# Performance work log

Measured on AMD Instinct MI355X. Metric: run time of the kernel, lower is better.

Reference implementation:

```python
import jax, jax.numpy as jnp
import numpy as np

N_ITEMS = 80001
D = 128
K = 20
HOP = 2
ROUTING_ITER = 4
SAMPLE = 12
B = 256
S = 50


def layer_norm(x, g, b, eps=1e-5):
    mu = jnp.mean(x, -1, keepdims=True)
    var = jnp.var(x, -1, keepdims=True)
    return (x - mu) * jax.lax.rsqrt(var + eps) * g + b


def routing_agg(x, nb0):
    # NeighborRoutingAgg (DisenGCN-style neighbor routing): x [N,d], nb0 [N,m] 0-based neighbor ids into x
    xn = x * jax.lax.rsqrt(jnp.sum(x * x, -1, keepdims=True) + 1e-12)
    z = xn[nb0]  # [N, m, d] irregular gather
    u = xn
    for _ in range(ROUTING_ITER):
        p = jax.nn.softmax(jnp.einsum('nd,nmd->nm', u, z), axis=1)
        u = xn + jnp.einsum('nm,nmd->nd', p, z)
        u = u * jax.lax.rsqrt(jnp.sum(u * u, -1, keepdims=True) + 1e-12)
    return u


def gru(x, W_ih, W_hh, b_ih, b_hh):
    # PyTorch nn.GRU, 1 layer, batch_first; x [B,S,d]
    Bb, Ss, d = x.shape
    h0 = jnp.zeros((Bb, d), x.dtype)
    gi_all = jnp.einsum('bsd,ed->bse', x, W_ih) + b_ih  # [B,S,3d] precompute input gates
    def step(h, gi):
        gh = h @ W_hh.T + b_hh
        i_r, i_z, i_n = jnp.split(gi, 3, -1)
        h_r, h_z, h_n = jnp.split(gh, 3, -1)
        r = jax.nn.sigmoid(i_r + h_r)
        zg = jax.nn.sigmoid(i_z + h_z)
        n = jnp.tanh(i_n + r * h_n)
        return (1.0 - zg) * n + zg * h, (1.0 - zg) * n + zg * h
    _, H = jax.lax.scan(step, h0, jnp.swapaxes(gi_all, 0, 1))
    return jnp.swapaxes(H, 0, 1)


def setup_inputs() -> dict:
    key = jax.random.key(0)
    ks = jax.random.split(key, 16)
    inp = {}
    inp['inp_sess'] = jax.random.randint(ks[0], (B, S), 0, N_ITEMS)
    inp['lengths'] = jax.random.randint(ks[1], (B,), 1, S + 1)
    inp['mask_inf'] = jnp.zeros((B, S), jnp.float32)
    inp['mask_1'] = jnp.ones((B, S), jnp.float32)
    inp['tau'] = jnp.float32(1.0)
    inp['adj_items'] = jax.random.randint(ks[2], (N_ITEMS, SAMPLE), 1, N_ITEMS)
    inp['anchors'] = jax.random.randint(ks[3], (K,), 1, N_ITEMS)
    inp['emb'] = jax.random.normal(ks[4], (N_ITEMS, D), jnp.float32) * 0.05
    inp['W_ih'] = jax.random.normal(ks[5], (3 * D, D), jnp.float32) * 0.05
    inp['W_hh'] = jax.random.normal(ks[6], (3 * D, D), jnp.float32) * 0.05
    inp['b_ih'] = jnp.zeros((3 * D,), jnp.float32)
    inp['b_hh'] = jnp.zeros((3 * D,), jnp.float32)
    inp['W1'] = jax.random.normal(ks[7], (D, D), jnp.float32) * 0.05
    inp['b1'] = jnp.zeros((D,), jnp.float32)
    inp['W2'] = jax.random.normal(ks[8], (K, D), jnp.float32) * 0.05
    inp['b2'] = jnp.zeros((K,), jnp.float32)
    inp['a1'] = jax.random.normal(ks[9], (1,), jnp.float32)
    inp['a2'] = jax.random.normal(ks[10], (1,), jnp.float32)
    for i, nm in enumerate(['ln1', 'ln2', 'ln3', 'ln4']):
        inp[nm + '_g'] = jnp.ones((D,), jnp.float32)
        inp[nm + '_b'] = jnp.zeros((D,), jnp.float32)
    return inp


def reference(inp_sess, lengths, mask_inf, mask_1, tau, adj_items, anchors, emb,
              W_ih, W_hh, b_ih, b_hh, W1, b1, W2, b2, a1, a2,
              ln1_g, ln1_b, ln2_g, ln2_b, ln3_g, ln3_b, ln4_g, ln4_b):
    # mask_inf / mask_1 are accepted by the torch forward but unused
    x = emb[1:]                       # [N-1, d] real items
    nb0 = adj_items[1:] - 1           # 0-based neighbor ids into x
    out = x
    acc = x
    for _ in range(HOP):
        out = routing_agg(out, nb0)
        acc = acc + out
    item_vectors = layer_norm(acc, ln1_g, ln1_b)          # [N-1, d]
    h = jax.nn.leaky_relu(item_vectors @ W1.T + b1)
    item_pop_prob = jax.nn.softmax((h @ W2.T + b2) / tau, axis=1)  # [N-1, K]
    anchors_emb = item_vectors[anchors - 1]               # [K, d]
    item_pop_vec = layer_norm(item_pop_prob @ anchors_emb, ln2_g, ln2_b)
    pad = jnp.zeros((1, D), item_vectors.dtype)
    iv = jnp.concatenate([pad, item_vectors], 0)          # [N, d]
    pv = jnp.concatenate([pad, item_pop_vec], 0)
    inp_emb = iv[inp_sess]                                # [B,S,d] (dropout off / eval)
    inp_pop = pv[inp_sess]
    H = layer_norm(gru(inp_emb, W_ih, W_hh, b_ih, b_hh), ln3_g, ln3_b)
    ht = H[jnp.arange(H.shape[0]), lengths - 1]           # [B, d]
    Hp = layer_norm(gru(inp_pop, W_ih, W_hh, b_ih, b_hh), ln4_g, ln4_b)
    ht_pop = Hp[jnp.arange(Hp.shape[0]), lengths - 1]
    scores_item = ht @ item_vectors.T                     # [B, N-1]
    scores_pop = ht_pop @ item_pop_vec.T
    scores = jax.nn.sigmoid(a1) * scores_item + jax.nn.sigmoid(a2) * scores_pop
    return scores, scores_item, scores_pop
```

## Files before the change

kernel.cpp:

```cpp
#include <hip/hip_runtime.h>

typedef unsigned short u16;
typedef unsigned int u32;
typedef __attribute__((ext_vector_type(8))) short short8;
typedef __attribute__((ext_vector_type(4))) float f32x4;

#define N_IT 80000
#define SLOT 10240000

__device__ __forceinline__ float wred(float v) {
#pragma unroll
    for (int s = 32; s; s >>= 1) v += __shfl_xor(v, s);
    return v;
}
__device__ __forceinline__ float sigf(float x) { return 1.f / (1.f + expf(-x)); }
__device__ __forceinline__ u16 f2bf(float f) {
    u32 x = __float_as_uint(f);
    u32 r = x + 0x7fffu + ((x >> 16) & 1u);
    return (u16)(r >> 16);
}
__device__ __forceinline__ float bf2f(u16 v) {
    return __uint_as_float(((u32)v) << 16);
}
__device__ __forceinline__ u32 pack2(float lo, float hi) {
    return ((u32)f2bf(hi) << 16) | f2bf(lo);
}
__device__ __forceinline__ f32x4 mfma16(short8 a, short8 b, f32x4 c) {
    return __builtin_amdgcn_mfma_f32_16x16x32_bf16(a, b, c, 0, 0, 0);
}
#define SWZ(v, pat) __int_as_float(__builtin_amdgcn_ds_swizzle(__float_as_int(v), pat))
__device__ __forceinline__ float red16(float t) {
    t += SWZ(t, 0x041F);
    t += SWZ(t, 0x081F);
    t += SWZ(t, 0x101F);
    t += SWZ(t, 0x201F);
    return t;
}
__device__ __forceinline__ float red16max(float t) {
    t = fmaxf(t, SWZ(t, 0x041F));
    t = fmaxf(t, SWZ(t, 0x081F));
    t = fmaxf(t, SWZ(t, 0x101F));
    t = fmaxf(t, SWZ(t, 0x201F));
    return t;
}
__device__ __forceinline__ float dot4(float4 a, float4 b) {
    return a.x * b.x + a.y * b.y + a.z * b.z + a.w * b.w;
}
__device__ __forceinline__ void unp8(uint4 w, float4& a, float4& b) {
    a.x = __uint_as_float(w.x << 16); a.y = __uint_as_float(w.x & 0xFFFF0000u);
    a.z = __uint_as_float(w.y << 16); a.w = __uint_as_float(w.y & 0xFFFF0000u);
    b.x = __uint_as_float(w.z << 16); b.y = __uint_as_float(w.z & 0xFFFF0000u);
    b.z = __uint_as_float(w.w << 16); b.w = __uint_as_float(w.w & 0xFFFF0000u);
}

__global__ __launch_bounds__(256) void k_cvtall(const float* __restrict__ Wih,
                                                const float* __restrict__ W1,
                                                const float* __restrict__ W2,
                                                u16* __restrict__ wihbf,
                                                u16* __restrict__ w1bf,
                                                u16* __restrict__ w2bf) {
    int i = blockIdx.x * 256 + threadIdx.x;
    if (i < 49152) {
        wihbf[i] = f2bf(Wih[i]);
    } else if (i < 65536) {
        int j = i - 49152;
        w1bf[j] = f2bf(W1[j]);
    } else if (i < 69632) {
        int j = i - 65536;
        int row = j >> 7, col = j & 127;
        w2bf[j] = (row < 20) ? f2bf(W2[row * 128 + col]) : (u16)0;
    }
}

__global__ __launch_bounds__(256) void k_prep(const int* __restrict__ anchors,
                                              const u16* __restrict__ ivbf,
                                              u16* __restrict__ anchT) {
    for (int e = threadIdx.x; e < 4096; e += 256) {
        int d = e >> 5, k = e & 31;
        anchT[e] = (k < 20) ? ivbf[(size_t)(anchors[k] - 1) * 128 + d] : (u16)0;
    }
}

__global__ __launch_bounds__(256) void k_normb(const float* __restrict__ x,
                                               u32* __restrict__ xn) {
    int wid = (blockIdx.x * blockDim.x + threadIdx.x) >> 6;
    int l = threadIdx.x & 63;
    size_t base = (size_t)wid * 128;
    float2 v = *(const float2*)(x + base + 2 * l);
    float s = wred(v.x * v.x + v.y * v.y);
    float r = 1.f / sqrtf(s + 1e-12f);
    xn[(size_t)wid * 64 + l] = pack2(v.x * r, v.y * r);
}

__global__ __launch_bounds__(256, 2) void k_routeb(const u32* __restrict__ xn,
                                                   const int* __restrict__ adj,
                                                   u32* __restrict__ out) {
    int tid = blockIdx.x * 256 + threadIdx.x;
    int item = tid >> 4;
    int sl = threadIdx.x & 15;
    float4 x0, x1;
    unp8(*(const uint4*)(xn + (size_t)item * 64 + sl * 4), x0, x1);
    const int4* ar = (const int4*)(adj + (size_t)(item + 1) * 12);
    int4 a0 = ar[0], a1 = ar[1], a2 = ar[2];
    float4 z0[12], z1[12];
#define LDZ(i, comp)                                                              \
    unp8(*(const uint4*)(xn + (size_t)((comp) - 1) * 64 + sl * 4), z0[i], z1[i]);
    LDZ(0, a0.x) LDZ(1, a0.y) LDZ(2, a0.z) LDZ(3, a0.w)
    LDZ(4, a1.x) LDZ(5, a1.y) LDZ(6, a1.z) LDZ(7, a1.w)
    LDZ(8, a2.x) LDZ(9, a2.y) LDZ(10, a2.z) LDZ(11, a2.w)
#undef LDZ
    float4 u0 = x0, u1 = x1;
#pragma unroll
    for (int it = 0; it < 4; it++) {
        float p[12]; float sum = 0.f;
#pragma unroll
        for (int m = 0; m < 12; m++) {
            float t = dot4(u0, z0[m]) + dot4(u1, z1[m]);
            t = red16(t);
            p[m] = __expf(t);
            sum += p[m];
        }
        float inv = 1.f / sum;
        u0 = x0; u1 = x1;
#pragma unroll
        for (int m = 0; m < 12; m++) {
            float pm = p[m] * inv;
            u0.x += pm * z0[m].x; u0.y += pm * z0[m].y;
            u0.z += pm * z0[m].z; u0.w += pm * z0[m].w;
            u1.x += pm * z1[m].x; u1.y += pm * z1[m].y;
            u1.z += pm * z1[m].z; u1.w += pm * z1[m].w;
        }
        float nn = red16(dot4(u0, u0) + dot4(u1, u1));
        float rr = 1.f / sqrtf(nn + 1e-12f);
        u0.x *= rr; u0.y *= rr; u0.z *= rr; u0.w *= rr;
        u1.x *= rr; u1.y *= rr; u1.z *= rr; u1.w *= rr;
    }
    uint4 o = make_uint4(pack2(u0.x, u0.y), pack2(u0.z, u0.w),
                         pack2(u1.x, u1.y), pack2(u1.z, u1.w));
    *(uint4*)(out + (size_t)item * 64 + sl * 4) = o;
}

__global__ __launch_bounds__(256, 2) void k_route2lnb(const u32* __restrict__ xn,
                                                      const float* __restrict__ emb,
                                                      const int* __restrict__ adj,
                                                      const float* __restrict__ g,
                                                      const float* __restrict__ bb,
                                                      u32* __restrict__ ivbf) {
    int tid = blockIdx.x * 256 + threadIdx.x;
    int item = tid >> 4;
    int sl = threadIdx.x & 15;
    float4 x0, x1;
    unp8(*(const uint4*)(xn + (size_t)item * 64 + sl * 4), x0, x1);
    const int4* ar = (const int4*)(adj + (size_t)(item + 1) * 12);
    int4 a0 = ar[0], a1 = ar[1], a2 = ar[2];
    float4 z0[12], z1[12];
#define LDZ(i, comp)                                                              \
    unp8(*(const uint4*)(xn + (size_t)((comp) - 1) * 64 + sl * 4), z0[i], z1[i]);
    LDZ(0, a0.x) LDZ(1, a0.y) LDZ(2, a0.z) LDZ(3, a0.w)
    LDZ(4, a1.x) LDZ(5, a1.y) LDZ(6, a1.z) LDZ(7, a1.w)
    LDZ(8, a2.x) LDZ(9, a2.y) LDZ(10, a2.z) LDZ(11, a2.w)
#undef LDZ
    float4 u0 = x0, u1 = x1;
#pragma unroll
    for (int it = 0; it < 4; it++) {
        float p[12]; float sum = 0.f;
#pragma unroll
        for (int m = 0; m < 12; m++) {
            float t = dot4(u0, z0[m]) + dot4(u1, z1[m]);
            t = red16(t);
            p[m] = __expf(t);
            sum += p[m];
        }
        float inv = 1.f / sum;
        u0 = x0; u1 = x1;
#pragma unroll
        for (int m = 0; m < 12; m++) {
            float pm = p[m] * inv;
            u0.x += pm * z0[m].x; u0.y += pm * z0[m].y;
            u0.z += pm * z0[m].z; u0.w += pm * z0[m].w;
            u1.x += pm * z1[m].x; u1.y += pm * z1[m].y;
            u1.z += pm * z1[m].z; u1.w += pm * z1[m].w;
        }
        float nn = red16(dot4(u0, u0) + dot4(u1, u1));
        float rr = 1.f / sqrtf(nn + 1e-12f);
        u0.x *= rr; u0.y *= rr; u0.z *= rr; u0.w *= rr;
        u1.x *= rr; u1.y *= rr; u1.z *= rr; u1.w *= rr;
    }
    const float4* er = (const float4*)(emb + (size_t)item * 128 + sl * 8);
    float4 e0 = er[0], e1 = er[1];
    float v[8];
    v[0] = e0.x + x0.x + u0.x; v[1] = e0.y + x0.y + u0.y;
    v[2] = e0.z + x0.z + u0.z; v[3] = e0.w + x0.w + u0.w;
    v[4] = e1.x + x1.x + u1.x; v[5] = e1.y + x1.y + u1.y;
    v[6] = e1.z + x1.z + u1.z; v[7] = e1.w + x1.w + u1.w;
    float s = 0.f, q = 0.f;
#pragma unroll
    for (int j = 0; j < 8; j++) { s += v[j]; q += v[j] * v[j]; }
    s = red16(s); q = red16(q);
    float mean = s * (1.f / 128.f);
    float var = q * (1.f / 128.f) - mean * mean;
    float r = 1.f / sqrtf(var + 1e-5f);
    const float4* gr = (const float4*)(g + sl * 8);
    const float4* br = (const float4*)(bb + sl * 8);
    float4 g0 = gr[0], g1 = gr[1], bw0 = br[0], bw1 = br[1];
    float y[8];
    y[0] = (v[0] - mean) * r * g0.x + bw0.x; y[1] = (v[1] - mean) * r * g0.y + bw0.y;
    y[2] = (v[2] - mean) * r * g0.z + bw0.z; y[3] = (v[3] - mean) * r * g0.w + bw0.w;
    y[4] = (v[4] - mean) * r * g1.x + bw1.x; y[5] = (v[5] - mean) * r * g1.y + bw1.y;
    y[6] = (v[6] - mean) * r * g1.z + bw1.z; y[7] = (v[7] - mean) * r * g1.w + bw1.w;
    uint4 o = make_uint4(pack2(y[0], y[1]), pack2(y[2], y[3]),
                         pack2(y[4], y[5]), pack2(y[6], y[7]));
    *(uint4*)(ivbf + (size_t)item * 64 + sl * 4) = o;
}

__global__ __launch_bounds__(256, 2) void k_popm(const u16* __restrict__ ivbf,
                                                 const u16* __restrict__ w1bf,
                                                 const float* __restrict__ b1,
                                                 const u16* __restrict__ w2bf,
                                                 const float* __restrict__ b2,
                                                 const float* __restrict__ tau,
                                                 const u16* __restrict__ anchT,
                                                 const float* __restrict__ g2,
                                                 const float* __restrict__ bb2,
                                                 u16* __restrict__ pvbf) {
    __shared__ u16 buf[4][16][136];
    int w = threadIdx.x >> 6, l = threadIdx.x & 63;
    int g16 = l >> 4, c = l & 15;
    int item0 = blockIdx.x * 64 + w * 16;
    const u16* ap = ivbf + (size_t)(item0 + c) * 128 + g16 * 8;
    short8 A[4];
#pragma unroll
    for (int kb = 0; kb < 4; kb++) A[kb] = *(const short8*)(ap + kb * 32);
#pragma unroll
    for (int nt = 0; nt < 8; nt++) {
        const u16* wp = w1bf + (nt * 16 + c) * 128 + g16 * 8;
        f32x4 acc = {0.f, 0.f, 0.f, 0.f};
#pragma unroll
        for (int kb = 0; kb < 4; kb++)
            acc = mfma16(A[kb], *(const short8*)(wp + kb * 32), acc);
        float bias = b1[nt * 16 + c];
#pragma unroll
        for (int qq = 0; qq < 4; qq++) {
            float hv = acc[qq] + bias;
            hv = hv >= 0.f ? hv : 0.01f * hv;
            buf[w][4 * g16 + qq][nt * 16 + c] = f2bf(hv);
        }
    }
    short8 A2[4];
#pragma unroll
    for (int kb = 0; kb < 4; kb++)
        A2[kb] = *(const short8*)&buf[w][c][g16 * 8 + kb * 32];
    f32x4 L0 = {0.f, 0.f, 0.f, 0.f}, L1 = {0.f, 0.f, 0.f, 0.f};
#pragma unroll
    for (int kb = 0; kb < 4; kb++) {
        L0 = mfma16(A2[kb], *(const short8*)(w2bf + c * 128 + g16 * 8 + kb * 32), L0);
        L1 = mfma16(A2[kb], *(const short8*)(w2bf + (16 + c) * 128 + g16 * 8 + kb * 32), L1);
    }
    float it = 1.f / tau[0];
    float b2v0 = b2[c];
    float b2v1 = (c < 4) ? b2[16 + c] : 0.f;
#pragma unroll
    for (int qq = 0; qq < 4; qq++) {
        float v0 = (L0[qq] + b2v0) * it;
        float v1 = (c < 4) ? (L1[qq] + b2v1) * it : -1e30f;
        float mx = red16max(fmaxf(v0, v1));
        float e0 = __expf(v0 - mx);
        float e1 = (c < 4) ? __expf(v1 - mx) : 0.f;
        float ssum = red16(e0 + e1);
        float inv = 1.f / ssum;
        buf[w][4 * g16 + qq][c] = f2bf(e0 * inv);
        buf[w][4 * g16 + qq][16 + c] = f2bf(e1 * inv);
    }
    short8 A3 = *(const short8*)&buf[w][c][g16 * 8];
    f32x4 pv[8];
#pragma unroll
    for (int nt = 0; nt < 8; nt++) {
        const short8 B3 = *(const short8*)(anchT + (nt * 16 + c) * 32 + g16 * 8);
        f32x4 zz = {0.f, 0.f, 0.f, 0.f};
        pv[nt] = mfma16(A3, B3, zz);
    }
    float g2v[8], b2gv[8];
#pragma unroll
    for (int t = 0; t < 8; t++) { g2v[t] = g2[t * 16 + c]; b2gv[t] = bb2[t * 16 + c]; }
#pragma unroll
    for (int qq = 0; qq < 4; qq++) {
        float ps = 0.f, psq = 0.f;
#pragma unroll
        for (int t = 0; t < 8; t++) { float x = pv[t][qq]; ps += x; psq += x * x; }
        float s = red16(ps), sq = red16(psq);
        float mean = s * (1.f / 128.f);
        float var = sq * (1.f / 128.f) - mean * mean;
        float r = 1.f / sqrtf(var + 1e-5f);
        size_t base = (size_t)(item0 + 4 * g16 + qq) * 128;
#pragma unroll
        for (int t = 0; t < 8; t++) {
            float y = (pv[t][qq] - mean) * r * g2v[t] + b2gv[t];
            pvbf[base + t * 16 + c] = f2bf(y);
        }
    }
}

__global__ __launch_bounds__(256) void k_gi(const int* __restrict__ sess,
                                            const u16* __restrict__ ivbf,
                                            const u16* __restrict__ pvbf,
                                            const u16* __restrict__ wbf,
                                            const float* __restrict__ bih,
                                            float* __restrict__ gi) {
    int w = threadIdx.x >> 6, l = threadIdx.x & 63;
    int mt = blockIdx.x * 4 + w;
    int r = mt * 16 + (l & 15);
    int s = r / 50, t = r - s * 50;
    int idx = sess[(s & 255) * 50 + t];
    const u16* srcb = (s < 256) ? ivbf : pvbf;
    int ko = (l >> 4) * 8;
    const short8 Z8 = {0, 0, 0, 0, 0, 0, 0, 0};
    short8 A[4];
    if (idx == 0) {
#pragma unroll
        for (int kb = 0; kb < 4; kb++) A[kb] = Z8;
    } else {
        const u16* rp = srcb + (size_t)(idx - 1) * 128 + ko;
#pragma unroll
        for (int kb = 0; kb < 4; kb++) A[kb] = *(const short8*)(rp + kb * 32);
    }
    int rowb = mt * 16 + (l >> 4) * 4;
    for (int nt = 0; nt < 24; nt++) {
        int gcol = nt * 16 + (l & 15);
        const u16* wp = wbf + gcol * 128 + ko;
        f32x4 acc = {0.f, 0.f, 0.f, 0.f};
#pragma unroll
        for (int kb = 0; kb < 4; kb++)
            acc = mfma16(A[kb], *(const short8*)(wp + kb * 32), acc);
        float bias = bih[gcol];
#pragma unroll
        for (int q = 0; q < 4; q++)
            gi[(size_t)(rowb + q) * 384 + gcol] = acc[q] + bias;
    }
}

__global__ __launch_bounds__(384, 2) void k_gru(const float* __restrict__ gi,
                                                const float* __restrict__ whh,
                                                const float* __restrict__ bhh,
                                                const int* __restrict__ lengths,
                                                const float* __restrict__ g3,
                                                const float* __restrict__ b3,
                                                const float* __restrict__ g4,
                                                const float* __restrict__ b4,
                                                u32* __restrict__ htbf) {
    __shared__ __align__(16) float hS[2][128];
    __shared__ float rS[128], zS[128], hnS[128], inS[128];
    int g = threadIdx.x, b = blockIdx.x;
    float4 wv[32];
    const float4* wr = (const float4*)(whh + g * 128);
#pragma unroll
    for (int k = 0; k < 32; k++) wv[k] = wr[k];
    float bh = bhh[g];
    if (g < 128) hS[0][g] = 0.f;
    int len = lengths[b & 255];
    const float* giS = gi + (size_t)b * 50 * 384 + g;
    __syncthreads();
    int par = 0;
    for (int t = 0; t < len; t++) {
        float ga = giS[t * 384];
        float aA = bh;
#pragma unroll
        for (int k = 0; k < 32; k++) {
            float4 w4 = wv[k];
            float4 ha = *(const float4*)&hS[par][k * 4];
            aA += w4.x * ha.x + w4.y * ha.y + w4.z * ha.z + w4.w * ha.w;
        }
        if (g < 128) {
            rS[g] = sigf(ga + aA);
        } else if (g < 256) {
            zS[g - 128] = sigf(ga + aA);
        } else {
            inS[g - 256] = ga; hnS[g - 256] = aA;
        }
        __syncthreads();
        if (g < 128) {
            float n = tanhf(inS[g] + rS[g] * hnS[g]);
            hS[par ^ 1][g] = (1.f - zS[g]) * n + zS[g] * hS[par][g];
        }
        __syncthreads();
        par ^= 1;
    }
    if (g < 64) {
        const float* lg = (b < 256) ? g3 : g4;
        const float* lb = (b < 256) ? b3 : b4;
        float2 v = *(const float2*)&hS[par][2 * g];
        float s = wred(v.x + v.y), q = wred(v.x * v.x + v.y * v.y);
        float mean = s * (1.f / 128.f), var = q * (1.f / 128.f) - mean * mean;
        float r = 1.f / sqrtf(var + 1e-5f);
        float2 gg = *(const float2*)(lg + 2 * g), bg = *(const float2*)(lb + 2 * g);
        float y0 = (v.x - mean) * r * gg.x + bg.x;
        float y1 = (v.y - mean) * r * gg.y + bg.y;
        htbf[(size_t)b * 64 + g] = ((u32)f2bf(y1) << 16) | f2bf(y0);
    }
}

__global__ __launch_bounds__(256) void k_scores(const u16* __restrict__ htbf,
                                                const u16* __restrict__ ivbf,
                                                const u16* __restrict__ pvbf,
                                                const float* __restrict__ a1,
                                                const float* __restrict__ a2,
                                                float* __restrict__ out) {
    int w = threadIdx.x >> 6, l = threadIdx.x & 63;
    int n0 = blockIdx.x * 64;
    int ko = (l >> 4) * 8;
    short8 Ai[4][4], Ap[4][4];
#pragma unroll
    for (int mi = 0; mi < 4; mi++) {
        int row = w * 64 + mi * 16 + (l & 15);
        const u16* pi = htbf + row * 128 + ko;
        const u16* pp = htbf + (row + 256) * 128 + ko;
#pragma unroll
        for (int kb = 0; kb < 4; kb++) {
            Ai[mi][kb] = *(const short8*)(pi + kb * 32);
            Ap[mi][kb] = *(const short8*)(pp + kb * 32);
        }
    }
    float s1 = sigf(a1[0]), s2 = sigf(a2[0]);
    float* sc = out;
    float* si = out + (size_t)20480000;
    float* sp = out + (size_t)40960000;
    for (int nt = 0; nt < 4; nt++) {
        int col = n0 + nt * 16 + (l & 15);
        const u16* bi = ivbf + (size_t)col * 128 + ko;
        const u16* bp = pvbf + (size_t)col * 128 + ko;
        short8 Bi[4], Bp[4];
#pragma unroll
        for (int kb = 0; kb < 4; kb++) {
            Bi[kb] = *(const short8*)(bi + kb * 32);
            Bp[kb] = *(const short8*)(bp + kb * 32);
        }
#pragma unroll
        for (int mi = 0; mi < 4; mi++) {
            f32x4 ai = {0.f, 0.f, 0.f, 0.f}, ap = {0.f, 0.f, 0.f, 0.f};
#pragma unroll
            for (int kb = 0; kb < 4; kb++) {
                ai = mfma16(Ai[mi][kb], Bi[kb], ai);
                ap = mfma16(Ap[mi][kb], Bp[kb], ap);
            }
            int rowb = w * 64 + mi * 16 + (l >> 4) * 4;
#pragma unroll
            for (int q = 0; q < 4; q++) {
                size_t o = (size_t)(rowb + q) * 80000 + col;
                float vi = ai[q], vp = ap[q];
                si[o] = vi;
                sp[o] = vp;
                sc[o] = s1 * vi + s2 * vp;
            }
        }
    }
}

extern "C" void kernel_launch(void* const* d_in, const int* in_sizes, int n_in,
                              void* d_out, int out_size, void* d_ws, size_t ws_size,
                              hipStream_t stream) {
    (void)in_sizes; (void)n_in; (void)out_size; (void)ws_size;
    const int*   sess    = (const int*)d_in[0];
    const int*   lengths = (const int*)d_in[1];
    const float* tau     = (const float*)d_in[4];
    const int*   adj     = (const int*)d_in[5];
    const int*   anchors = (const int*)d_in[6];
    const float* emb     = (const float*)d_in[7];
    const float* W_ih    = (const float*)d_in[8];
    const float* W_hh    = (const float*)d_in[9];
    const float* b_ih    = (const float*)d_in[10];
    const float* b_hh    = (const float*)d_in[11];
    const float* W1      = (const float*)d_in[12];
    const float* b1      = (const float*)d_in[13];
    const float* W2      = (const float*)d_in[14];
    const float* b2      = (const float*)d_in[15];
    const float* a1      = (const float*)d_in[16];
    const float* a2      = (const float*)d_in[17];
    const float* ln1g = (const float*)d_in[18];
    const float* ln1b = (const float*)d_in[19];
    const float* ln2g = (const float*)d_in[20];
    const float* ln2b = (const float*)d_in[21];
    const float* ln3g = (const float*)d_in[22];
    const float* ln3b = (const float*)d_in[23];
    const float* ln4g = (const float*)d_in[24];
    const float* ln4b = (const float*)d_in[25];

    float* out = (float*)d_out;
    u32*   o_xn = (u32*)out;
    u32*   o_o1 = (u32*)(out + SLOT);
    float* o_gi = out + 2 * SLOT;

    u16* ws16   = (u16*)d_ws;
    u16* ivbf   = ws16;
    u16* pvbf   = ws16 + 10240000;
    u16* wihbf  = ws16 + 20480000;
    u16* htbf   = ws16 + 20529152;
    u16* w1bf   = ws16 + 20594688;
    u16* w2bf   = ws16 + 20611072;
    u16* anchT  = ws16 + 20615168;

    k_cvtall<<<272, 256, 0, stream>>>(W_ih, W1, W2, wihbf, w1bf, w2bf);
    k_normb<<<20000, 256, 0, stream>>>(emb + 128, o_xn);
    k_routeb<<<5000, 256, 0, stream>>>(o_xn, adj, o_o1);
    k_route2lnb<<<5000, 256, 0, stream>>>(o_o1, emb + 128, adj, ln1g, ln1b, (u32*)ivbf);
    k_prep<<<1, 256, 0, stream>>>(anchors, ivbf, anchT);
    k_popm<<<1250, 256, 0, stream>>>(ivbf, w1bf, b1, w2bf, b2, tau, anchT,
                                     ln2g, ln2b, pvbf);
    k_gi<<<400, 256, 0, stream>>>(sess, ivbf, pvbf, wihbf, b_ih, o_gi);
    k_gru<<<512, 384, 0, stream>>>(o_gi, W_hh, b_hh, lengths, ln3g, ln3b, ln4g, ln4b,
                                   (u32*)htbf);
    k_scores<<<1250, 256, 0, stream>>>(htbf, ivbf, pvbf, a1, a2, out);
}
```

Before: 429.1 us.

## Fuse small prep kernels, keep routing neighbors packed, store gi as bf16, nontemporal score writes

Merges the weight-conversion and normalization kernels into one launch and folds the anchor-transpose kernel into k_popm via shared memory, removing two launches. The routing kernels now keep the 12 gathered neighbor rows as packed bf16 and unpack them on use, which cuts register pressure so occupancy can rise from 2 to 3 blocks per CU. The GRU input-gate buffer is stored as bf16 to halve its traffic, and the large score outputs use nontemporal stores. These changes cost extra unpack ALU work, redundant anchor gathers in every popm block, and some precision in the gate inputs.

```diff
diff --git a/kernel.cpp b/kernel.cpp
--- a/kernel.cpp
+++ b/kernel.cpp
@@ -53,37 +53,29 @@
     b.z = __uint_as_float(w.w << 16); b.w = __uint_as_float(w.w & 0xFFFF0000u);
 }
 
-__global__ __launch_bounds__(256) void k_cvtall(const float* __restrict__ Wih,
-                                                const float* __restrict__ W1,
-                                                const float* __restrict__ W2,
-                                                u16* __restrict__ wihbf,
-                                                u16* __restrict__ w1bf,
-                                                u16* __restrict__ w2bf) {
-    int i = blockIdx.x * 256 + threadIdx.x;
-    if (i < 49152) {
-        wihbf[i] = f2bf(Wih[i]);
-    } else if (i < 65536) {
-        int j = i - 49152;
-        w1bf[j] = f2bf(W1[j]);
-    } else if (i < 69632) {
-        int j = i - 65536;
-        int row = j >> 7, col = j & 127;
-        w2bf[j] = (row < 20) ? f2bf(W2[row * 128 + col]) : (u16)0;
-    }
-}
-
-__global__ __launch_bounds__(256) void k_prep(const int* __restrict__ anchors,
-                                              const u16* __restrict__ ivbf,
-                                              u16* __restrict__ anchT) {
-    for (int e = threadIdx.x; e < 4096; e += 256) {
-        int d = e >> 5, k = e & 31;
-        anchT[e] = (k < 20) ? ivbf[(size_t)(anchors[k] - 1) * 128 + d] : (u16)0;
-    }
-}
-
-__global__ __launch_bounds__(256) void k_normb(const float* __restrict__ x,
-                                               u32* __restrict__ xn) {
-    int wid = (blockIdx.x * blockDim.x + threadIdx.x) >> 6;
+__global__ __launch_bounds__(256) void k_cvtnorm(const float* __restrict__ Wih,
+                                                 const float* __restrict__ W1,
+                                                 const float* __restrict__ W2,
+                                                 u16* __restrict__ wihbf,
+                                                 u16* __restrict__ w1bf,
+                                                 u16* __restrict__ w2bf,
+                                                 const float* __restrict__ x,
+                                                 u32* __restrict__ xn) {
+    if (blockIdx.x < 272) {
+        int i = blockIdx.x * 256 + threadIdx.x;
+        if (i < 49152) {
+            wihbf[i] = f2bf(Wih[i]);
+        } else if (i < 65536) {
+            int j = i - 49152;
+            w1bf[j] = f2bf(W1[j]);
+        } else if (i < 69632) {
+            int j = i - 65536;
+            int row = j >> 7, col = j & 127;
+            w2bf[j] = (row < 20) ? f2bf(W2[row * 128 + col]) : (u16)0;
+        }
+        return;
+    }
+    int wid = ((blockIdx.x - 272) * 256 + threadIdx.x) >> 6;
     int l = threadIdx.x & 63;
     size_t base = (size_t)wid * 128;
     float2 v = *(const float2*)(x + base + 2 * l);
@@ -92,7 +84,7 @@
     xn[(size_t)wid * 64 + l] = pack2(v.x * r, v.y * r);
 }
 
-__global__ __launch_bounds__(256, 2) void k_routeb(const u32* __restrict__ xn,
+__global__ __launch_bounds__(256, 3) void k_routeb(const u32* __restrict__ xn,
                                                    const int* __restrict__ adj,
                                                    u32* __restrict__ out) {
     int tid = blockIdx.x * 256 + threadIdx.x;
@@ -102,9 +94,8 @@
     unp8(*(const uint4*)(xn + (size_t)item * 64 + sl * 4), x0, x1);
     const int4* ar = (const int4*)(adj + (size_t)(item + 1) * 12);
     int4 a0 = ar[0], a1 = ar[1], a2 = ar[2];
-    float4 z0[12], z1[12];
-#define LDZ(i, comp)                                                              \
-    unp8(*(const uint4*)(xn + (size_t)((comp) - 1) * 64 + sl * 4), z0[i], z1[i]);
+    uint4 zw[12];
+#define LDZ(i, comp) zw[i] = *(const uint4*)(xn + (size_t)((comp) - 1) * 64 + sl * 4);
     LDZ(0, a0.x) LDZ(1, a0.y) LDZ(2, a0.z) LDZ(3, a0.w)
     LDZ(4, a1.x) LDZ(5, a1.y) LDZ(6, a1.z) LDZ(7, a1.w)
     LDZ(8, a2.x) LDZ(9, a2.y) LDZ(10, a2.z) LDZ(11, a2.w)
@@ -115,7 +106,8 @@
         float p[12]; float sum = 0.f;
 #pragma unroll
         for (int m = 0; m < 12; m++) {
-            float t = dot4(u0, z0[m]) + dot4(u1, z1[m]);
+            float4 a, b; unp8(zw[m], a, b);
+            float t = dot4(u0, a) + dot4(u1, b);
             t = red16(t);
             p[m] = __expf(t);
             sum += p[m];
@@ -125,10 +117,9 @@
 #pragma unroll
         for (int m = 0; m < 12; m++) {
             float pm = p[m] * inv;
-            u0.x += pm * z0[m].x; u0.y += pm * z0[m].y;
-            u0.z += pm * z0[m].z; u0.w += pm * z0[m].w;
-            u1.x += pm * z1[m].x; u1.y += pm * z1[m].y;
-            u1.z += pm * z1[m].z; u1.w += pm * z1[m].w;
+            float4 a, b; unp8(zw[m], a, b);
+            u0.x += pm * a.x; u0.y += pm * a.y; u0.z += pm * a.z; u0.w += pm * a.w;
+            u1.x += pm * b.x; u1.y += pm * b.y; u1.z += pm * b.z; u1.w += pm * b.w;
         }
         float nn = red16(dot4(u0, u0) + dot4(u1, u1));
         float rr = 1.f / sqrtf(nn + 1e-12f);
@@ -140,7 +131,7 @@
     *(uint4*)(out + (size_t)item * 64 + sl * 4) = o;
 }
 
-__global__ __launch_bounds__(256, 2) void k_route2lnb(const u32* __restrict__ xn,
+__global__ __launch_bounds__(256, 3) void k_route2lnb(const u32* __restrict__ xn,
                                                       const float* __restrict__ emb,
                                                       const int* __restrict__ adj,
                                                       const float* __restrict__ g,
@@ -153,9 +144,8 @@
     unp8(*(const uint4*)(xn + (size_t)item * 64 + sl * 4), x0, x1);
     const int4* ar = (const int4*)(adj + (size_t)(item + 1) * 12);
     int4 a0 = ar[0], a1 = ar[1], a2 = ar[2];
-    float4 z0[12], z1[12];
-#define LDZ(i, comp)                                                              \
-    unp8(*(const uint4*)(xn + (size_t)((comp) - 1) * 64 + sl * 4), z0[i], z1[i]);
+    uint4 zw[12];
+#define LDZ(i, comp) zw[i] = *(const uint4*)(xn + (size_t)((comp) - 1) * 64 + sl * 4);
     LDZ(0, a0.x) LDZ(1, a0.y) LDZ(2, a0.z) LDZ(3, a0.w)
     LDZ(4, a1.x) LDZ(5, a1.y) LDZ(6, a1.z) LDZ(7, a1.w)
     LDZ(8, a2.x) LDZ(9, a2.y) LDZ(10, a2.z) LDZ(11, a2.w)
@@ -166,7 +156,8 @@
         float p[12]; float sum = 0.f;
 #pragma unroll
         for (int m = 0; m < 12; m++) {
-            float t = dot4(u0, z0[m]) + dot4(u1, z1[m]);
+            float4 a, b; unp8(zw[m], a, b);
+            float t = dot4(u0, a) + dot4(u1, b);
             t = red16(t);
             p[m] = __expf(t);
             sum += p[m];
@@ -176,10 +167,9 @@
 #pragma unroll
         for (int m = 0; m < 12; m++) {
             float pm = p[m] * inv;
-            u0.x += pm * z0[m].x; u0.y += pm * z0[m].y;
-            u0.z += pm * z0[m].z; u0.w += pm * z0[m].w;
-            u1.x += pm * z1[m].x; u1.y += pm * z1[m].y;
-            u1.z += pm * z1[m].z; u1.w += pm * z1[m].w;
+            float4 a, b; unp8(zw[m], a, b);
+            u0.x += pm * a.x; u0.y += pm * a.y; u0.z += pm * a.z; u0.w += pm * a.w;
+            u1.x += pm * b.x; u1.y += pm * b.y; u1.z += pm * b.z; u1.w += pm * b.w;
         }
         float nn = red16(dot4(u0, u0) + dot4(u1, u1));
         float rr = 1.f / sqrtf(nn + 1e-12f);
@@ -219,12 +209,19 @@
                                                  const u16* __restrict__ w2bf,
                                                  const float* __restrict__ b2,
                                                  const float* __restrict__ tau,
-                                                 const u16* __restrict__ anchT,
+                                                 const int* __restrict__ anchors,
                                                  const float* __restrict__ g2,
                                                  const float* __restrict__ bb2,
                                                  u16* __restrict__ pvbf) {
     __shared__ u16 buf[4][16][136];
-    int w = threadIdx.x >> 6, l = threadIdx.x & 63;
+    __shared__ u16 anchS[128][40];
+    int tid = threadIdx.x;
+    for (int e = tid; e < 4096; e += 256) {
+        int d = e >> 5, k = e & 31;
+        anchS[d][k] = (k < 20) ? ivbf[(size_t)(anchors[k] - 1) * 128 + d] : (u16)0;
+    }
+    __syncthreads();
+    int w = tid >> 6, l = tid & 63;
     int g16 = l >> 4, c = l & 15;
     int item0 = blockIdx.x * 64 + w * 16;
     const u16* ap = ivbf + (size_t)(item0 + c) * 128 + g16 * 8;
@@ -275,7 +272,7 @@
     f32x4 pv[8];
 #pragma unroll
     for (int nt = 0; nt < 8; nt++) {
-        const short8 B3 = *(const short8*)(anchT + (nt * 16 + c) * 32 + g16 * 8);
+        const short8 B3 = *(const short8*)&anchS[nt * 16 + c][g16 * 8];
         f32x4 zz = {0.f, 0.f, 0.f, 0.f};
         pv[nt] = mfma16(A3, B3, zz);
     }
@@ -305,7 +302,7 @@
                                             const u16* __restrict__ pvbf,
                                             const u16* __restrict__ wbf,
                                             const float* __restrict__ bih,
-                                            float* __restrict__ gi) {
+                                            u16* __restrict__ gi) {
     int w = threadIdx.x >> 6, l = threadIdx.x & 63;
     int mt = blockIdx.x * 4 + w;
     int r = mt * 16 + (l & 15);
@@ -334,11 +331,11 @@
         float bias = bih[gcol];
 #pragma unroll
         for (int q = 0; q < 4; q++)
-            gi[(size_t)(rowb + q) * 384 + gcol] = acc[q] + bias;
-    }
-}
-
-__global__ __launch_bounds__(384, 2) void k_gru(const float* __restrict__ gi,
+            gi[(size_t)(rowb + q) * 384 + gcol] = f2bf(acc[q] + bias);
+    }
+}
+
+__global__ __launch_bounds__(384, 2) void k_gru(const u16* __restrict__ gi,
                                                 const float* __restrict__ whh,
                                                 const float* __restrict__ bhh,
                                                 const int* __restrict__ lengths,
@@ -357,11 +354,11 @@
     float bh = bhh[g];
     if (g < 128) hS[0][g] = 0.f;
     int len = lengths[b & 255];
-    const float* giS = gi + (size_t)b * 50 * 384 + g;
+    const u16* giS = gi + (size_t)b * 50 * 384 + g;
     __syncthreads();
     int par = 0;
     for (int t = 0; t < len; t++) {
-        float ga = giS[t * 384];
+        float ga = bf2f(giS[t * 384]);
         float aA = bh;
 #pragma unroll
         for (int k = 0; k < 32; k++) {
@@ -446,9 +443,9 @@
             for (int q = 0; q < 4; q++) {
                 size_t o = (size_t)(rowb + q) * 80000 + col;
                 float vi = ai[q], vp = ap[q];
-                si[o] = vi;
-                sp[o] = vp;
-                sc[o] = s1 * vi + s2 * vp;
+                __builtin_nontemporal_store(vi, si + o);
+                __builtin_nontemporal_store(vp, sp + o);
+                __builtin_nontemporal_store(s1 * vi + s2 * vp, sc + o);
             }
         }
     }
@@ -484,9 +481,9 @@
     const float* ln4b = (const float*)d_in[25];
 
     float* out = (float*)d_out;
-    u32*   o_xn = (u32*)out;
-    u32*   o_o1 = (u32*)(out + SLOT);
-    float* o_gi = out + 2 * SLOT;
+    u32* o_xn = (u32*)out;
+    u32* o_o1 = (u32*)(out + SLOT);
+    u16* o_gi = (u16*)(out + 2 * SLOT);
 
     u16* ws16   = (u16*)d_ws;
     u16* ivbf   = ws16;
@@ -495,14 +492,12 @@
     u16* htbf   = ws16 + 20529152;
     u16* w1bf   = ws16 + 20594688;
     u16* w2bf   = ws16 + 20611072;
-    u16* anchT  = ws16 + 20615168;
-
-    k_cvtall<<<272, 256, 0, stream>>>(W_ih, W1, W2, wihbf, w1bf, w2bf);
-    k_normb<<<20000, 256, 0, stream>>>(emb + 128, o_xn);
+
+    k_cvtnorm<<<20272, 256, 0, stream>>>(W_ih, W1, W2, wihbf, w1bf, w2bf,
+                                         emb + 128, o_xn);
     k_routeb<<<5000, 256, 0, stream>>>(o_xn, adj, o_o1);
     k_route2lnb<<<5000, 256, 0, stream>>>(o_o1, emb + 128, adj, ln1g, ln1b, (u32*)ivbf);
-    k_prep<<<1, 256, 0, stream>>>(anchors, ivbf, anchT);
-    k_popm<<<1250, 256, 0, stream>>>(ivbf, w1bf, b1, w2bf, b2, tau, anchT,
+    k_popm<<<1250, 256, 0, stream>>>(ivbf, w1bf, b1, w2bf, b2, tau, anchors,
                                      ln2g, ln2b, pvbf);
     k_gi<<<400, 256, 0, stream>>>(sess, ivbf, pvbf, wihbf, b_ih, o_gi);
     k_gru<<<512, 384, 0, stream>>>(o_gi, W_hh, b_hh, lengths, ln3g, ln3b, ln4g, ln4b,
```

New measurement: 662.9 us. 1.54x slower.
